# Kernel optimization log

Measured on AMD Instinct MI355X. Metric: run time of the kernel, lower is better.

The kernel has to match this reference:

```python
import jax, jax.numpy as jnp
import numpy as np
from jax import lax

# ---- dims / config (see init_kwargs) ----
M_IMG, N_PCD, C = 1008, 1024, 256     # coarse img nodes (24*32+12*16+6*8), coarse pcd nodes, feat dim
NI_F, NP_F = 76800, 30000             # fine img pixels (240*320), fine pcd points
KI, KP = 64, 64                       # knn patch sizes
NUM_CORR, TOPK = 256, 3               # coarse matching params
COARSE_THR, FINE_THR = 0.0, 0.0       # similarity thresholds (lowered for random data)


def _norm(x):
    return x / (jnp.linalg.norm(x, axis=-1, keepdims=True) + 1e-8)


def setup_inputs() -> dict:
    key = jax.random.key(0)
    ks = jax.random.split(key, 7)
    return {
        "img_feats_c": _norm(jax.random.normal(ks[0], (M_IMG, C), jnp.float32)),
        "pcd_feats_c": _norm(jax.random.normal(ks[1], (N_PCD, C), jnp.float32)),
        "img_feats_f": _norm(jax.random.normal(ks[2], (NI_F, C), jnp.float32)),
        "pcd_feats_f": _norm(jax.random.normal(ks[3], (NP_F, C), jnp.float32)),
        "img_node_masks": jnp.ones((M_IMG,), bool),
        "pcd_node_masks": jnp.ones((N_PCD,), bool),
        "img_node_knn_indices": jax.random.randint(ks[4], (M_IMG, KI), 0, NI_F),
        "pcd_node_knn_indices": jax.random.randint(ks[5], (N_PCD, KP), 0, NP_F),
        "pcd_node_knn_masks": jax.random.uniform(ks[6], (N_PCD, KP)) > 0.1,
    }


def _coarse_match(img_feats_c, pcd_feats_c, img_masks, pcd_masks):
    # SuperPointMatchingMutualTopk: cosine sim + mutual top-k + global top NUM_CORR
    sim = img_feats_c @ pcd_feats_c.T                              # [M, N] (feats normalized)
    valid = img_masks[:, None] & pcd_masks[None, :]
    sim_m = jnp.where(valid, sim, -jnp.inf)
    row_kth = lax.top_k(sim_m, TOPK)[0][:, -1:]                    # kth-largest per row [M,1]
    col_kth = lax.top_k(sim_m.T, TOPK)[0][:, -1:].T                # kth-largest per col [1,N]
    mutual = (sim_m >= row_kth) & (sim_m >= col_kth) & (sim_m > COARSE_THR)
    flat = jnp.where(mutual, sim_m, -jnp.inf).ravel()
    vals, flat_idx = lax.top_k(flat, NUM_CORR)                     # fixed-size selection
    img_idx = flat_idx // N_PCD
    pcd_idx = flat_idx % N_PCD
    corr_valid = jnp.isfinite(vals)
    return img_idx, pcd_idx, corr_valid


def reference(img_feats_c, pcd_feats_c, img_feats_f, pcd_feats_f,
              img_node_masks, pcd_node_masks,
              img_node_knn_indices, pcd_node_knn_indices, pcd_node_knn_masks):
    # ---- coarse matching ----
    img_idx, pcd_idx, corr_valid = _coarse_match(
        img_feats_c, pcd_feats_c, img_node_masks, pcd_node_masks)

    # ---- fine matching: knn gather + pairwise cosine + mutual top-1 ----
    pcd_padded = jnp.concatenate([pcd_feats_f, jnp.zeros_like(pcd_feats_f[:1])], axis=0)
    img_knn_idx = img_node_knn_indices[img_idx]                    # [Ci, KI]
    pcd_knn_idx = pcd_node_knn_indices[pcd_idx]                    # [Ci, KP]
    pcd_knn_msk = pcd_node_knn_masks[pcd_idx]                      # [Ci, KP]
    img_knn_feats = img_feats_f[img_knn_idx]                       # [Ci, KI, C]
    pcd_knn_feats = pcd_padded[pcd_knn_idx]                        # [Ci, KP, C]

    sim = jnp.einsum('bic,bjc->bij', img_knn_feats, pcd_knn_feats) # [Ci, KI, KP]
    m3 = corr_valid[:, None, None] & pcd_knn_msk[:, None, :]
    sim = jnp.where(m3, sim, -jnp.inf)

    row_best = jnp.argmax(sim, axis=2)                             # [Ci, KI]
    row_val = jnp.max(sim, axis=2)
    col_best = jnp.argmax(sim, axis=1)                             # [Ci, KP]
    back = jnp.take_along_axis(col_best, row_best, axis=1)         # [Ci, KI]
    sel = (back == jnp.arange(KI)[None, :]) & jnp.isfinite(row_val) & (row_val > FINE_THR)

    img_corr = img_knn_idx.reshape(-1)                             # [Ci*KI]
    pcd_corr = jnp.take_along_axis(pcd_knn_idx, row_best, axis=1).reshape(-1)
    sel = sel.reshape(-1)
    # sentinel for unselected pairs -> sorts last
    img_corr = jnp.where(sel, img_corr, NI_F)
    pcd_corr = jnp.where(sel, pcd_corr, NP_F)

    # ---- dedup (torch.unique on img*Npf+pcd) via lexsort + first-occurrence mask ----
    order = jnp.lexsort((pcd_corr, img_corr))
    ic, pc = img_corr[order], pcd_corr[order]
    first = jnp.concatenate([jnp.array([True]),
                             (ic[1:] != ic[:-1]) | (pc[1:] != pc[:-1])])
    valid = first & (ic < NI_F)

    ic_s = jnp.clip(ic, 0, NI_F - 1)
    pc_s = jnp.clip(pc, 0, NP_F - 1)
    corr_scores = jnp.sum(img_feats_f[ic_s] * pcd_feats_f[pc_s], axis=1)
    corr_scores = corr_scores * valid.astype(corr_scores.dtype)    # masked scores [Ci*KI]
    return corr_scores
```

## Files before the change

kernel.cpp:

```cpp
#include <hip/hip_runtime.h>
#include <hip/hip_bf16.h>

#define M_IMG 1008
#define N_PCD 1024
#define CDIM  256
#define NI_F  76800
#define NP_F  30000
#define KI    64
#define KP    64
#define NUM_CORR 256
#define NPAIR (NUM_CORR * KI)
#define CAND_CAP 4096
#define KEY_MOD 30001u
#define SENT_KEY (76800u * 30001u + 30000u)

#define NCHUNK 21
#define NEG_INF (-__builtin_inff())

__device__ __forceinline__ bool mask_val(const void* p, int i, int is_u8) {
    return is_u8 ? (((const unsigned char*)p)[i] != 0)
                 : (((const int*)p)[i] != 0);
}

__global__ void detect_bool_kernel(const unsigned int* __restrict__ p,
                                   int* __restrict__ flag) {
    __shared__ int s_cnt;
    if (threadIdx.x == 0) s_cnt = 0;
    __syncthreads();
    unsigned int x = p[blockIdx.x * 256 + threadIdx.x];
    if (x & 0xFFFFFF00u) atomicAdd(&s_cnt, 1);
    __syncthreads();
    if (threadIdx.x == 0 && s_cnt != 0) atomicAdd(flag, 1);
}


__global__ void coarse_sim_kernel(const float* __restrict__ A,
                                  const float* __restrict__ B,
                                  const void* __restrict__ maskA,
                                  const void* __restrict__ maskB,
                                  const int* __restrict__ flag,
                                  float* __restrict__ sim) {
    __shared__ __align__(16) float s_a[32][36];
    __shared__ __align__(16) float s_b[32][68];
    const int is_u8 = (*flag != 0);
    const int m0 = blockIdx.y * 32, n0 = blockIdx.x * 64;
    const int tid = threadIdx.x;
    const int tx = tid & 15, ty = tid >> 4;
    const int c_lane = tid & 31;
    const int r_base = tid >> 5;

    const float* pa[4];
    const float* pb[8];
#pragma unroll
    for (int k = 0; k < 4; k++) {
        int m = m0 + r_base + 8 * k;
        pa[k] = A + (size_t)(m < M_IMG ? m : 0) * CDIM + c_lane;
    }
#pragma unroll
    for (int k = 0; k < 8; k++)
        pb[k] = B + (size_t)(n0 + r_base + 8 * k) * CDIM + c_lane;

    float ra[4], rb[8];
#pragma unroll
    for (int k = 0; k < 4; k++) ra[k] = pa[k][0];
#pragma unroll
    for (int k = 0; k < 8; k++) rb[k] = pb[k][0];
#pragma unroll
    for (int k = 0; k < 4; k++) s_a[c_lane][r_base + 8 * k] = ra[k];
#pragma unroll
    for (int k = 0; k < 8; k++) s_b[c_lane][r_base + 8 * k] = rb[k];
    __syncthreads();

    float acc[2][4];
#pragma unroll
    for (int r = 0; r < 2; r++)
#pragma unroll
        for (int j = 0; j < 4; j++) acc[r][j] = 0.f;

    for (int cit = 0; cit < 8; cit++) {
        if (cit < 7) {
            const int cc = (cit + 1) * 32;
#pragma unroll
            for (int k = 0; k < 4; k++) ra[k] = pa[k][cc];
#pragma unroll
            for (int k = 0; k < 8; k++) rb[k] = pb[k][cc];
        }
#pragma unroll 8
        for (int c = 0; c < 32; c++) {
            float2 av = *(const float2*)&s_a[c][ty * 2];
            float4 bv = *(const float4*)&s_b[c][tx * 4];
            float ar[2] = {av.x, av.y};
            float br[4] = {bv.x, bv.y, bv.z, bv.w};
#pragma unroll
            for (int r = 0; r < 2; r++)
#pragma unroll
                for (int j = 0; j < 4; j++) acc[r][j] += ar[r] * br[j];
        }
        __syncthreads();
        if (cit < 7) {
#pragma unroll
            for (int k = 0; k < 4; k++) s_a[c_lane][r_base + 8 * k] = ra[k];
#pragma unroll
            for (int k = 0; k < 8; k++) s_b[c_lane][r_base + 8 * k] = rb[k];
            __syncthreads();
        }
    }
#pragma unroll
    for (int r = 0; r < 2; r++) {
        int m = m0 + ty * 2 + r;
        if (m < M_IMG) {
            bool ma = mask_val(maskA, m, is_u8);
#pragma unroll
            for (int j = 0; j < 4; j++) {
                int n = n0 + tx * 4 + j;
                bool ok = ma && mask_val(maskB, n, is_u8);
                sim[m * N_PCD + n] = ok ? acc[r][j] : NEG_INF;
            }
        }
    }
}

__device__ __forceinline__ void top3_insert(float v, float& t0, float& t1, float& t2) {
    if (v > t0) { t2 = t1; t1 = t0; t0 = v; }
    else if (v > t1) { t2 = t1; t1 = v; }
    else if (v > t2) { t2 = v; }
}

__device__ __forceinline__ void top3_merge(float a0, float a1, float a2,
                                           float b0, float b1, float b2,
                                           float& x0, float& x1, float& x2) {
    if (a0 >= b0) {
        x0 = a0;
        if (a1 >= b0) { x1 = a1; x2 = (a2 >= b0) ? a2 : b0; }
        else          { x1 = b0; x2 = (a1 >= b1) ? a1 : b1; }
    } else {
        x0 = b0;
        if (b1 >= a0) { x1 = b1; x2 = (b2 >= a0) ? b2 : a0; }
        else          { x1 = a0; x2 = (b1 >= a1) ? b1 : a1; }
    }
}

__global__ void kth_kernel(const float* __restrict__ sim,
                           float* __restrict__ row_kth,
                           float* __restrict__ colp) {
    __shared__ float st[256][3];
    const int tid = threadIdx.x;
    if (blockIdx.x < M_IMG) {
        const float* r = sim + (size_t)blockIdx.x * N_PCD;
        float t0 = NEG_INF, t1 = NEG_INF, t2 = NEG_INF;
#pragma unroll
        for (int e = 0; e < 4; e++) top3_insert(r[e * 256 + tid], t0, t1, t2);
        st[tid][0] = t0; st[tid][1] = t1; st[tid][2] = t2;
        __syncthreads();
        for (int s = 128; s > 0; s >>= 1) {
            if (tid < s) {
                float x0, x1, x2;
                top3_merge(st[tid][0], st[tid][1], st[tid][2],
                           st[tid + s][0], st[tid + s][1], st[tid + s][2],
                           x0, x1, x2);
                st[tid][0] = x0; st[tid][1] = x1; st[tid][2] = x2;
            }
            __syncthreads();
        }
        if (tid == 0) row_kth[blockIdx.x] = st[0][2];
    } else {
        const int b = blockIdx.x - M_IMG;
        const int bx = b & 15, by = b >> 4;
        const int c = tid & 63, rr = tid >> 6;
        const int col = bx * 64 + c;
        const int r0 = by * 48;
        float t0 = NEG_INF, t1 = NEG_INF, t2 = NEG_INF;
#pragma unroll
        for (int k = 0; k < 12; k++) {
            float v = sim[(size_t)(r0 + rr + 4 * k) * N_PCD + col];
            top3_insert(v, t0, t1, t2);
        }
        st[tid][0] = t0; st[tid][1] = t1; st[tid][2] = t2;
        __syncthreads();
        if (tid < 128) {
            float x0, x1, x2;
            top3_merge(st[tid][0], st[tid][1], st[tid][2],
                       st[tid + 128][0], st[tid + 128][1], st[tid + 128][2],
                       x0, x1, x2);
            st[tid][0] = x0; st[tid][1] = x1; st[tid][2] = x2;
        }
        __syncthreads();
        if (tid < 64) {
            float x0, x1, x2;
            top3_merge(st[tid][0], st[tid][1], st[tid][2],
                       st[tid + 64][0], st[tid + 64][1], st[tid + 64][2],
                       x0, x1, x2);
            const int base = by * N_PCD + col;
            colp[base] = x0;
            colp[NCHUNK * N_PCD + base] = x1;
            colp[2 * NCHUNK * N_PCD + base] = x2;
        }
    }
}

__global__ void col_merge_kernel(const float* __restrict__ colp,
                                 float* __restrict__ col_kth) {
    const int col = blockIdx.x * 256 + threadIdx.x;
    float t0 = colp[col];
    float t1 = colp[NCHUNK * N_PCD + col];
    float t2 = colp[2 * NCHUNK * N_PCD + col];
#pragma unroll
    for (int ch = 1; ch < NCHUNK; ch++) {
        float b0 = colp[ch * N_PCD + col];
        float b1 = colp[NCHUNK * N_PCD + ch * N_PCD + col];
        float b2 = colp[2 * NCHUNK * N_PCD + ch * N_PCD + col];
        float x0, x1, x2;
        top3_merge(t0, t1, t2, b0, b1, b2, x0, x1, x2);
        t0 = x0; t1 = x1; t2 = x2;
    }
    col_kth[col] = t2;
}

__global__ void compact_kernel(const float* __restrict__ sim,
                               const float* __restrict__ row_kth,
                               const float* __restrict__ col_kth,
                               unsigned long long* __restrict__ cand,
                               int* __restrict__ count) {
    int g = blockIdx.x * 256 + threadIdx.x;
    if (g >= M_IMG * N_PCD) return;
    int m = g >> 10, n = g & 1023;
    float v = sim[g];
    if (v > 0.f && v >= row_kth[m] && v >= col_kth[n]) {
        int pos = atomicAdd(count, 1);
        if (pos < CAND_CAP) {
            unsigned int u = __float_as_uint(v);
            unsigned int mono = (u & 0x80000000u) ? ~u : (u | 0x80000000u);
            cand[pos] = ((unsigned long long)(~mono) << 32) | (unsigned int)g;
        }
    }
}

__global__ void cand_rank_kernel(const unsigned long long* __restrict__ cand,
                                 const int* __restrict__ count,
                                 unsigned int* __restrict__ cnt2) {
    __shared__ unsigned long long s_k[256];
    const int tid = threadIdx.x;
    int K = *count; if (K > CAND_CAP) K = CAND_CAP;
    const int j0 = blockIdx.y * 256;
    if (j0 >= K) return;
    int j = j0 + tid;
    s_k[tid] = (j < K) ? cand[j] : 0xFFFFFFFFFFFFFFFFull;
    __syncthreads();
    const int i = blockIdx.x * 256 + tid;
    if (i >= K) return;
    const unsigned long long my = cand[i];
    unsigned int less = 0;
#pragma unroll 8
    for (int t = 0; t < 256; t++) less += (s_k[t] < my);
    if (less) atomicAdd(&cnt2[i], less);
}

__global__ void cand_select_kernel(const unsigned long long* __restrict__ cand,
                                   const int* __restrict__ count,
                                   const unsigned int* __restrict__ cnt2,
                                   int* __restrict__ sel_idx,
                                   int* __restrict__ selK) {
    int K = *count; if (K > CAND_CAP) K = CAND_CAP;
    const int i = blockIdx.x * 256 + threadIdx.x;
    if (i == 0) *selK = (K < NUM_CORR) ? K : NUM_CORR;
    if (i < K) {
        unsigned int r = cnt2[i];
        if (r < NUM_CORR) sel_idx[r] = (int)(cand[i] & 0xFFFFFFFFull);
    }
}

__global__ void fine_kernel(const float* __restrict__ img_f,
                            const float* __restrict__ pcd_f,
                            const int* __restrict__ img_knn,
                            const int* __restrict__ pcd_knn,
                            const void* __restrict__ pcd_msk,
                            const int* __restrict__ flag,
                            const int* __restrict__ sel_idx,
                            const int* __restrict__ selK_ptr,
                            unsigned int* __restrict__ keys) {
    const int ci = blockIdx.x, tid = threadIdx.x;
    const int selK = *selK_ptr;
    if (ci >= selK) {
        if (tid < KI) keys[ci * KI + tid] = SENT_KEY;
        return;
    }
    __shared__ int s_ik[KI], s_pk[KP];
    __shared__ unsigned char s_mk[KP];
    __shared__ __align__(16) float s_a[32][68];
    __shared__ __align__(16) float s_b[32][68];
    __shared__ float s_sim[64][65];
    __shared__ int s_rb[64], s_cb[64];
    __shared__ float s_rv[64];

    int flat = sel_idx[ci];
    int gi = flat >> 10, pi = flat & 1023;
    if (tid < 64) {
        const int is_u8 = (*flag != 0);
        s_ik[tid] = img_knn[gi * KI + tid];
        s_pk[tid] = pcd_knn[pi * KP + tid];
        s_mk[tid] = mask_val(pcd_msk, pi * KP + tid, is_u8) ? 1 : 0;
    }
    __syncthreads();

    const int tx = tid & 15, tyy = tid >> 4;
    const int c_lane = tid & 31;
    const int r_base = tid >> 5;

    const float* pa[4];
    const float* pb[4];
#pragma unroll
    for (int k = 0; k < 4; k++) {
        pa[k] = img_f + (size_t)s_ik[r_base + 16 * k] * CDIM + c_lane;
        pb[k] = pcd_f + (size_t)s_pk[r_base + 16 * k] * CDIM + c_lane;
    }

    float ra[4], rb[4];
#pragma unroll
    for (int k = 0; k < 4; k++) { ra[k] = pa[k][0]; rb[k] = pb[k][0]; }
#pragma unroll
    for (int k = 0; k < 4; k++) {
        s_a[c_lane][r_base + 16 * k] = ra[k];
        s_b[c_lane][r_base + 16 * k] = rb[k];
    }
    __syncthreads();

    float acc[2][4];
#pragma unroll
    for (int r = 0; r < 2; r++)
#pragma unroll
        for (int j = 0; j < 4; j++) acc[r][j] = 0.f;

    for (int cit = 0; cit < 8; cit++) {
        if (cit < 7) {
            const int cc = (cit + 1) * 32;
#pragma unroll
            for (int k = 0; k < 4; k++) { ra[k] = pa[k][cc]; rb[k] = pb[k][cc]; }
        }
#pragma unroll 8
        for (int c = 0; c < 32; c++) {
            float2 av = *(const float2*)&s_a[c][tyy * 2];
            float4 bv = *(const float4*)&s_b[c][tx * 4];
            float ar[2] = {av.x, av.y};
            float br[4] = {bv.x, bv.y, bv.z, bv.w};
#pragma unroll
            for (int r = 0; r < 2; r++)
#pragma unroll
                for (int j = 0; j < 4; j++) acc[r][j] += ar[r] * br[j];
        }
        __syncthreads();
        if (cit < 7) {
#pragma unroll
            for (int k = 0; k < 4; k++) {
                s_a[c_lane][r_base + 16 * k] = ra[k];
                s_b[c_lane][r_base + 16 * k] = rb[k];
            }
            __syncthreads();
        }
    }
#pragma unroll
    for (int r = 0; r < 2; r++) {
        int row = tyy * 2 + r;
#pragma unroll
        for (int j = 0; j < 4; j++) {
            int kp = tx * 4 + j;
            s_sim[row][kp] = (s_mk[kp] != 0) ? acc[r][j] : NEG_INF;
        }
    }
    __syncthreads();

    if (tid < 64) {
        float best = NEG_INF; int bi = 0;
        for (int kp = 0; kp < 64; kp++) {
            float v = s_sim[tid][kp];
            if (v > best) { best = v; bi = kp; }
        }
        s_rb[tid] = bi; s_rv[tid] = best;
    } else if (tid < 128) {
        int kp = tid - 64;
        float best = NEG_INF; int bi = 0;
        for (int k2 = 0; k2 < 64; k2++) {
            float v = s_sim[k2][kp];
            if (v > best) { best = v; bi = k2; }
        }
        s_cb[kp] = bi;
    }
    __syncthreads();

    if (tid < 64) {
        int rb2 = s_rb[tid];
        float rv = s_rv[tid];
        bool sel = (s_cb[rb2] == tid) && (rv > 0.f);
        unsigned int key = sel
            ? ((unsigned int)s_ik[tid] * KEY_MOD + (unsigned int)s_pk[rb2])
            : SENT_KEY;
        keys[ci * KI + tid] = key;
    }
}

__global__ void rank_count_kernel(const unsigned int* __restrict__ keys,
                                  unsigned int* __restrict__ cnt) {
    __shared__ unsigned int s_k[256];
    const int tid = threadIdx.x;
    const int bi = blockIdx.x, bj = blockIdx.y;
    const int i = bi * 256 + tid;
    const unsigned int myKey = keys[i];
    s_k[tid] = keys[bj * 256 + tid];
    __syncthreads();

    unsigned int less = 0, eqb = 0;
    if (bj < bi) {
#pragma unroll 8
        for (int j = 0; j < 256; j++) {
            unsigned int k = s_k[j];
            less += (k < myKey);
            eqb += (k == myKey);
        }
    } else if (bj == bi) {
#pragma unroll 8
        for (int j = 0; j < 256; j++) {
            unsigned int k = s_k[j];
            less += (k < myKey);
            eqb += (k == myKey) & (j < tid);
        }
    } else {
#pragma unroll 8
        for (int j = 0; j < 256; j++) {
            unsigned int k = s_k[j];
            less += (k < myKey);
        }
    }
    atomicAdd(&cnt[i], (less << 16) | eqb);
}

__global__ void rank_out_kernel(const unsigned int* __restrict__ keys,
                                const unsigned int* __restrict__ cnt,
                                const float* __restrict__ img_f,
                                const float* __restrict__ pcd_f,
                                float* __restrict__ out) {
    const int i = blockIdx.x * 256 + threadIdx.x;
    const unsigned int myKey = keys[i];
    const unsigned int v = cnt[i];
    const int rank = (int)(v >> 16) + (int)(v & 0xFFFFu);
    unsigned int ic = myKey / KEY_MOD;
    unsigned int pc = myKey - ic * KEY_MOD;
    float score = 0.f;
    if ((v & 0xFFFFu) == 0 && ic < (unsigned)NI_F) {
        const float4* a = (const float4*)(img_f + (size_t)ic * CDIM);
        const float4* b = (const float4*)(pcd_f + (size_t)pc * CDIM);
        float s = 0.f;
#pragma unroll 8
        for (int c = 0; c < CDIM / 4; c++) {
            float4 x = a[c], y = b[c];
            s += x.x * y.x + x.y * y.y + x.z * y.z + x.w * y.w;
        }
        score = s;
    }
    out[rank] = score;
}

extern "C" void kernel_launch(void* const* d_in, const int* in_sizes, int n_in,
                              void* d_out, int out_size, void* d_ws, size_t ws_size,
                              hipStream_t stream) {
    const float* img_c = (const float*)d_in[0];
    const float* pcd_c = (const float*)d_in[1];
    const float* img_f = (const float*)d_in[2];
    const float* pcd_f = (const float*)d_in[3];
    const void* img_mask = d_in[4];
    const void* pcd_mask = d_in[5];
    const int* img_knn = (const int*)d_in[6];
    const int* pcd_knn = (const int*)d_in[7];
    const void* pcd_knn_msk = d_in[8];
    float* out = (float*)d_out;

    char* w = (char*)d_ws;
    size_t off = 0;
    float* sim = (float*)(w + off);            off += (size_t)M_IMG * N_PCD * 4;
    float* row_kth = (float*)(w + off);        off += M_IMG * 4;
    float* col_kth = (float*)(w + off);        off += N_PCD * 4;
    int* count = (int*)(w + off);              off += 4;
    int* selK = (int*)(w + off);               off += 4;
    int* boolflag = (int*)(w + off);           off += 4;
    off = (off + 7) & ~(size_t)7;
    unsigned long long* cand = (unsigned long long*)(w + off); off += CAND_CAP * 8;
    int* sel_idx = (int*)(w + off);            off += NUM_CORR * 4;
    unsigned int* keys = (unsigned int*)(w + off); off += NPAIR * 4;
    unsigned int* cnt = (unsigned int*)(w + off);  off += NPAIR * 4;
    unsigned int* cnt2 = (unsigned int*)(w + off); off += CAND_CAP * 4;
    float* colp = (float*)(w + off);           off += 3 * NCHUNK * N_PCD * 4;

    hipMemsetAsync(count, 0, 12, stream);
    hipMemsetAsync(cnt, 0, (NPAIR + CAND_CAP) * 4, stream);

    detect_bool_kernel<<<16, 256, 0, stream>>>((const unsigned int*)pcd_knn_msk, boolflag);
    coarse_sim_kernel<<<dim3(16, 32), 256, 0, stream>>>(img_c, pcd_c, img_mask, pcd_mask,
                                                        boolflag, sim);
    kth_kernel<<<M_IMG + 16 * NCHUNK, 256, 0, stream>>>(sim, row_kth, colp);
    col_merge_kernel<<<4, 256, 0, stream>>>(colp, col_kth);
    compact_kernel<<<(M_IMG * N_PCD) / 256, 256, 0, stream>>>(sim, row_kth, col_kth, cand, count);
    cand_rank_kernel<<<dim3(16, 16), 256, 0, stream>>>(cand, count, cnt2);
    cand_select_kernel<<<16, 256, 0, stream>>>(cand, count, cnt2, sel_idx, selK);
    fine_kernel<<<NUM_CORR, 512, 0, stream>>>(img_f, pcd_f, img_knn, pcd_knn, pcd_knn_msk,
                                              boolflag, sel_idx, selK, keys);
    rank_count_kernel<<<dim3(64, 64), 256, 0, stream>>>(keys, cnt);
    rank_out_kernel<<<NPAIR / 256, 256, 0, stream>>>(keys, cnt, img_f, pcd_f, out);
}
```

Before: 274.1 us.

## Fuse row/column top-3 into sim GEMM and compact fine pairs before ranking

Computes per-tile row and column top-3 partials in the coarse similarity kernel's epilogue, so the separate kth kernel no longer has to re-read the whole sim matrix. A small kernel then merges the partials. Candidate ranking and selection are merged into one kernel, which removes the cnt2 buffer and its atomics. The fine kernel now appends only selected pairs to a compacted list, so the pairwise rank and output kernels work on valid entries only; in exchange the output must be zeroed by a memset and rank ties are broken by list position.

```diff
diff --git a/kernel.cpp b/kernel.cpp
--- a/kernel.cpp
+++ b/kernel.cpp
@@ -12,10 +12,9 @@
 #define NPAIR (NUM_CORR * KI)
 #define CAND_CAP 4096
 #define KEY_MOD 30001u
-#define SENT_KEY (76800u * 30001u + 30000u)
-
-#define NCHUNK 21
+
 #define NEG_INF (-__builtin_inff())
+typedef unsigned long long u64;
 
 __device__ __forceinline__ bool mask_val(const void* p, int i, int is_u8) {
     return is_u8 ? (((const unsigned char*)p)[i] != 0)
@@ -31,93 +30,6 @@
     if (x & 0xFFFFFF00u) atomicAdd(&s_cnt, 1);
     __syncthreads();
     if (threadIdx.x == 0 && s_cnt != 0) atomicAdd(flag, 1);
-}
-
-
-__global__ void coarse_sim_kernel(const float* __restrict__ A,
-                                  const float* __restrict__ B,
-                                  const void* __restrict__ maskA,
-                                  const void* __restrict__ maskB,
-                                  const int* __restrict__ flag,
-                                  float* __restrict__ sim) {
-    __shared__ __align__(16) float s_a[32][36];
-    __shared__ __align__(16) float s_b[32][68];
-    const int is_u8 = (*flag != 0);
-    const int m0 = blockIdx.y * 32, n0 = blockIdx.x * 64;
-    const int tid = threadIdx.x;
-    const int tx = tid & 15, ty = tid >> 4;
-    const int c_lane = tid & 31;
-    const int r_base = tid >> 5;
-
-    const float* pa[4];
-    const float* pb[8];
-#pragma unroll
-    for (int k = 0; k < 4; k++) {
-        int m = m0 + r_base + 8 * k;
-        pa[k] = A + (size_t)(m < M_IMG ? m : 0) * CDIM + c_lane;
-    }
-#pragma unroll
-    for (int k = 0; k < 8; k++)
-        pb[k] = B + (size_t)(n0 + r_base + 8 * k) * CDIM + c_lane;
-
-    float ra[4], rb[8];
-#pragma unroll
-    for (int k = 0; k < 4; k++) ra[k] = pa[k][0];
-#pragma unroll
-    for (int k = 0; k < 8; k++) rb[k] = pb[k][0];
-#pragma unroll
-    for (int k = 0; k < 4; k++) s_a[c_lane][r_base + 8 * k] = ra[k];
-#pragma unroll
-    for (int k = 0; k < 8; k++) s_b[c_lane][r_base + 8 * k] = rb[k];
-    __syncthreads();
-
-    float acc[2][4];
-#pragma unroll
-    for (int r = 0; r < 2; r++)
-#pragma unroll
-        for (int j = 0; j < 4; j++) acc[r][j] = 0.f;
-
-    for (int cit = 0; cit < 8; cit++) {
-        if (cit < 7) {
-            const int cc = (cit + 1) * 32;
-#pragma unroll
-            for (int k = 0; k < 4; k++) ra[k] = pa[k][cc];
-#pragma unroll
-            for (int k = 0; k < 8; k++) rb[k] = pb[k][cc];
-        }
-#pragma unroll 8
-        for (int c = 0; c < 32; c++) {
-            float2 av = *(const float2*)&s_a[c][ty * 2];
-            float4 bv = *(const float4*)&s_b[c][tx * 4];
-            float ar[2] = {av.x, av.y};
-            float br[4] = {bv.x, bv.y, bv.z, bv.w};
-#pragma unroll
-            for (int r = 0; r < 2; r++)
-#pragma unroll
-                for (int j = 0; j < 4; j++) acc[r][j] += ar[r] * br[j];
-        }
-        __syncthreads();
-        if (cit < 7) {
-#pragma unroll
-            for (int k = 0; k < 4; k++) s_a[c_lane][r_base + 8 * k] = ra[k];
-#pragma unroll
-            for (int k = 0; k < 8; k++) s_b[c_lane][r_base + 8 * k] = rb[k];
-            __syncthreads();
-        }
-    }
-#pragma unroll
-    for (int r = 0; r < 2; r++) {
-        int m = m0 + ty * 2 + r;
-        if (m < M_IMG) {
-            bool ma = mask_val(maskA, m, is_u8);
-#pragma unroll
-            for (int j = 0; j < 4; j++) {
-                int n = n0 + tx * 4 + j;
-                bool ok = ma && mask_val(maskB, n, is_u8);
-                sim[m * N_PCD + n] = ok ? acc[r][j] : NEG_INF;
-            }
-        }
-    }
 }
 
 __device__ __forceinline__ void top3_insert(float v, float& t0, float& t1, float& t2) {
@@ -140,86 +52,179 @@
     }
 }
 
-__global__ void kth_kernel(const float* __restrict__ sim,
-                           float* __restrict__ row_kth,
-                           float* __restrict__ colp) {
-    __shared__ float st[256][3];
+__global__ void coarse_sim_kernel(const float* __restrict__ A,
+                                  const float* __restrict__ B,
+                                  const void* __restrict__ maskA,
+                                  const void* __restrict__ maskB,
+                                  const int* __restrict__ flag,
+                                  float* __restrict__ sim,
+                                  float* __restrict__ rowp,
+                                  float* __restrict__ colp) {
+    __shared__ __align__(16) float s_a[32][36];
+    __shared__ __align__(16) float s_b[32][68];
+    __shared__ float sr[32][16][3];
+    __shared__ float sc[64][16][3];
+    const int is_u8 = (*flag != 0);
+    const int m0 = blockIdx.y * 32, n0 = blockIdx.x * 64;
     const int tid = threadIdx.x;
-    if (blockIdx.x < M_IMG) {
-        const float* r = sim + (size_t)blockIdx.x * N_PCD;
+    const int tx = tid & 15, ty = tid >> 4;
+    const int c_lane = tid & 31;
+    const int r_base = tid >> 5;
+
+    const float* pa[4];
+    const float* pb[8];
+#pragma unroll
+    for (int k = 0; k < 4; k++) {
+        int m = m0 + r_base + 8 * k;
+        pa[k] = A + (size_t)(m < M_IMG ? m : 0) * CDIM + c_lane;
+    }
+#pragma unroll
+    for (int k = 0; k < 8; k++)
+        pb[k] = B + (size_t)(n0 + r_base + 8 * k) * CDIM + c_lane;
+
+    float ra[4], rb[8];
+#pragma unroll
+    for (int k = 0; k < 4; k++) ra[k] = pa[k][0];
+#pragma unroll
+    for (int k = 0; k < 8; k++) rb[k] = pb[k][0];
+#pragma unroll
+    for (int k = 0; k < 4; k++) s_a[c_lane][r_base + 8 * k] = ra[k];
+#pragma unroll
+    for (int k = 0; k < 8; k++) s_b[c_lane][r_base + 8 * k] = rb[k];
+    __syncthreads();
+
+    float acc[2][4];
+#pragma unroll
+    for (int r = 0; r < 2; r++)
+#pragma unroll
+        for (int j = 0; j < 4; j++) acc[r][j] = 0.f;
+
+    for (int cit = 0; cit < 8; cit++) {
+        if (cit < 7) {
+            const int cc = (cit + 1) * 32;
+#pragma unroll
+            for (int k = 0; k < 4; k++) ra[k] = pa[k][cc];
+#pragma unroll
+            for (int k = 0; k < 8; k++) rb[k] = pb[k][cc];
+        }
+#pragma unroll 8
+        for (int c = 0; c < 32; c++) {
+            float2 av = *(const float2*)&s_a[c][ty * 2];
+            float4 bv = *(const float4*)&s_b[c][tx * 4];
+            float ar[2] = {av.x, av.y};
+            float br[4] = {bv.x, bv.y, bv.z, bv.w};
+#pragma unroll
+            for (int r = 0; r < 2; r++)
+#pragma unroll
+                for (int j = 0; j < 4; j++) acc[r][j] += ar[r] * br[j];
+        }
+        __syncthreads();
+        if (cit < 7) {
+#pragma unroll
+            for (int k = 0; k < 4; k++) s_a[c_lane][r_base + 8 * k] = ra[k];
+#pragma unroll
+            for (int k = 0; k < 8; k++) s_b[c_lane][r_base + 8 * k] = rb[k];
+            __syncthreads();
+        }
+    }
+
+    float vm[2][4];
+#pragma unroll
+    for (int r = 0; r < 2; r++) {
+        int m = m0 + ty * 2 + r;
+        bool ma = (m < M_IMG) && mask_val(maskA, m, is_u8);
+#pragma unroll
+        for (int j = 0; j < 4; j++) {
+            int n = n0 + tx * 4 + j;
+            bool ok = ma && mask_val(maskB, n, is_u8);
+            float v = ok ? acc[r][j] : NEG_INF;
+            vm[r][j] = v;
+            if (m < M_IMG) sim[m * N_PCD + n] = v;
+        }
+    }
+#pragma unroll
+    for (int r = 0; r < 2; r++) {
         float t0 = NEG_INF, t1 = NEG_INF, t2 = NEG_INF;
 #pragma unroll
-        for (int e = 0; e < 4; e++) top3_insert(r[e * 256 + tid], t0, t1, t2);
-        st[tid][0] = t0; st[tid][1] = t1; st[tid][2] = t2;
-        __syncthreads();
-        for (int s = 128; s > 0; s >>= 1) {
-            if (tid < s) {
-                float x0, x1, x2;
-                top3_merge(st[tid][0], st[tid][1], st[tid][2],
-                           st[tid + s][0], st[tid + s][1], st[tid + s][2],
-                           x0, x1, x2);
-                st[tid][0] = x0; st[tid][1] = x1; st[tid][2] = x2;
-            }
-            __syncthreads();
-        }
-        if (tid == 0) row_kth[blockIdx.x] = st[0][2];
+        for (int j = 0; j < 4; j++) top3_insert(vm[r][j], t0, t1, t2);
+        sr[ty * 2 + r][tx][0] = t0; sr[ty * 2 + r][tx][1] = t1; sr[ty * 2 + r][tx][2] = t2;
+    }
+#pragma unroll
+    for (int j = 0; j < 4; j++) {
+        float t0 = NEG_INF, t1 = NEG_INF, t2 = NEG_INF;
+        top3_insert(vm[0][j], t0, t1, t2);
+        top3_insert(vm[1][j], t0, t1, t2);
+        sc[tx * 4 + j][ty][0] = t0; sc[tx * 4 + j][ty][1] = t1; sc[tx * 4 + j][ty][2] = t2;
+    }
+    __syncthreads();
+    if (tid < 32) {
+        float t0 = sr[tid][0][0], t1 = sr[tid][0][1], t2 = sr[tid][0][2];
+#pragma unroll
+        for (int k = 1; k < 16; k++) {
+            float x0, x1, x2;
+            top3_merge(t0, t1, t2, sr[tid][k][0], sr[tid][k][1], sr[tid][k][2], x0, x1, x2);
+            t0 = x0; t1 = x1; t2 = x2;
+        }
+        int m = m0 + tid;
+        if (m < M_IMG) {
+            const int base = blockIdx.x * 1024 + m;
+            rowp[base] = t0;
+            rowp[16 * 1024 + base] = t1;
+            rowp[2 * 16 * 1024 + base] = t2;
+        }
+    } else if (tid >= 64 && tid < 128) {
+        int col = tid - 64;
+        float t0 = sc[col][0][0], t1 = sc[col][0][1], t2 = sc[col][0][2];
+#pragma unroll
+        for (int k = 1; k < 16; k++) {
+            float x0, x1, x2;
+            top3_merge(t0, t1, t2, sc[col][k][0], sc[col][k][1], sc[col][k][2], x0, x1, x2);
+            t0 = x0; t1 = x1; t2 = x2;
+        }
+        const int base = blockIdx.y * 1024 + n0 + col;
+        colp[base] = t0;
+        colp[32 * 1024 + base] = t1;
+        colp[2 * 32 * 1024 + base] = t2;
+    }
+}
+
+__global__ void kth_merge_kernel(const float* __restrict__ rowp,
+                                 const float* __restrict__ colp,
+                                 float* __restrict__ row_kth,
+                                 float* __restrict__ col_kth) {
+    const int b = blockIdx.x, t = threadIdx.x;
+    if (b < 4) {
+        int m = b * 256 + t;
+        if (m >= M_IMG) return;
+        float t0 = rowp[m], t1 = rowp[16 * 1024 + m], t2 = rowp[2 * 16 * 1024 + m];
+#pragma unroll
+        for (int ch = 1; ch < 16; ch++) {
+            int base = ch * 1024 + m;
+            float x0, x1, x2;
+            top3_merge(t0, t1, t2, rowp[base], rowp[16 * 1024 + base],
+                       rowp[2 * 16 * 1024 + base], x0, x1, x2);
+            t0 = x0; t1 = x1; t2 = x2;
+        }
+        row_kth[m] = t2;
     } else {
-        const int b = blockIdx.x - M_IMG;
-        const int bx = b & 15, by = b >> 4;
-        const int c = tid & 63, rr = tid >> 6;
-        const int col = bx * 64 + c;
-        const int r0 = by * 48;
-        float t0 = NEG_INF, t1 = NEG_INF, t2 = NEG_INF;
-#pragma unroll
-        for (int k = 0; k < 12; k++) {
-            float v = sim[(size_t)(r0 + rr + 4 * k) * N_PCD + col];
-            top3_insert(v, t0, t1, t2);
-        }
-        st[tid][0] = t0; st[tid][1] = t1; st[tid][2] = t2;
-        __syncthreads();
-        if (tid < 128) {
+        int n = (b - 4) * 256 + t;
+        float t0 = colp[n], t1 = colp[32 * 1024 + n], t2 = colp[2 * 32 * 1024 + n];
+#pragma unroll
+        for (int ch = 1; ch < 32; ch++) {
+            int base = ch * 1024 + n;
             float x0, x1, x2;
-            top3_merge(st[tid][0], st[tid][1], st[tid][2],
-                       st[tid + 128][0], st[tid + 128][1], st[tid + 128][2],
-                       x0, x1, x2);
-            st[tid][0] = x0; st[tid][1] = x1; st[tid][2] = x2;
-        }
-        __syncthreads();
-        if (tid < 64) {
-            float x0, x1, x2;
-            top3_merge(st[tid][0], st[tid][1], st[tid][2],
-                       st[tid + 64][0], st[tid + 64][1], st[tid + 64][2],
-                       x0, x1, x2);
-            const int base = by * N_PCD + col;
-            colp[base] = x0;
-            colp[NCHUNK * N_PCD + base] = x1;
-            colp[2 * NCHUNK * N_PCD + base] = x2;
-        }
-    }
-}
-
-__global__ void col_merge_kernel(const float* __restrict__ colp,
-                                 float* __restrict__ col_kth) {
-    const int col = blockIdx.x * 256 + threadIdx.x;
-    float t0 = colp[col];
-    float t1 = colp[NCHUNK * N_PCD + col];
-    float t2 = colp[2 * NCHUNK * N_PCD + col];
-#pragma unroll
-    for (int ch = 1; ch < NCHUNK; ch++) {
-        float b0 = colp[ch * N_PCD + col];
-        float b1 = colp[NCHUNK * N_PCD + ch * N_PCD + col];
-        float b2 = colp[2 * NCHUNK * N_PCD + ch * N_PCD + col];
-        float x0, x1, x2;
-        top3_merge(t0, t1, t2, b0, b1, b2, x0, x1, x2);
-        t0 = x0; t1 = x1; t2 = x2;
-    }
-    col_kth[col] = t2;
+            top3_merge(t0, t1, t2, colp[base], colp[32 * 1024 + base],
+                       colp[2 * 32 * 1024 + base], x0, x1, x2);
+            t0 = x0; t1 = x1; t2 = x2;
+        }
+        col_kth[n] = t2;
+    }
 }
 
 __global__ void compact_kernel(const float* __restrict__ sim,
                                const float* __restrict__ row_kth,
                                const float* __restrict__ col_kth,
-                               unsigned long long* __restrict__ cand,
+                               u64* __restrict__ cand,
                                int* __restrict__ count) {
     int g = blockIdx.x * 256 + threadIdx.x;
     if (g >= M_IMG * N_PCD) return;
@@ -230,43 +235,32 @@
         if (pos < CAND_CAP) {
             unsigned int u = __float_as_uint(v);
             unsigned int mono = (u & 0x80000000u) ? ~u : (u | 0x80000000u);
-            cand[pos] = ((unsigned long long)(~mono) << 32) | (unsigned int)g;
-        }
-    }
-}
-
-__global__ void cand_rank_kernel(const unsigned long long* __restrict__ cand,
-                                 const int* __restrict__ count,
-                                 unsigned int* __restrict__ cnt2) {
-    __shared__ unsigned long long s_k[256];
-    const int tid = threadIdx.x;
+            cand[pos] = ((u64)(~mono) << 32) | (unsigned int)g;
+        }
+    }
+}
+
+__global__ void cand_rank_select_kernel(const u64* __restrict__ cand,
+                                        const int* __restrict__ count,
+                                        int* __restrict__ sel_idx,
+                                        int* __restrict__ selK) {
+    __shared__ u64 s[256];
+    const int tid = threadIdx.x, bi = blockIdx.x;
     int K = *count; if (K > CAND_CAP) K = CAND_CAP;
-    const int j0 = blockIdx.y * 256;
-    if (j0 >= K) return;
-    int j = j0 + tid;
-    s_k[tid] = (j < K) ? cand[j] : 0xFFFFFFFFFFFFFFFFull;
-    __syncthreads();
-    const int i = blockIdx.x * 256 + tid;
-    if (i >= K) return;
-    const unsigned long long my = cand[i];
+    if (bi == 0 && tid == 0) *selK = (K < NUM_CORR) ? K : NUM_CORR;
+    if (bi * 256 >= K) return;
+    const int i = bi * 256 + tid;
+    const u64 my = (i < K) ? cand[i] : 0xFFFFFFFFFFFFFFFFull;
     unsigned int less = 0;
+    for (int c0 = 0; c0 < K; c0 += 256) {
+        int j = c0 + tid;
+        s[tid] = (j < K) ? cand[j] : 0xFFFFFFFFFFFFFFFFull;
+        __syncthreads();
 #pragma unroll 8
-    for (int t = 0; t < 256; t++) less += (s_k[t] < my);
-    if (less) atomicAdd(&cnt2[i], less);
-}
-
-__global__ void cand_select_kernel(const unsigned long long* __restrict__ cand,
-                                   const int* __restrict__ count,
-                                   const unsigned int* __restrict__ cnt2,
-                                   int* __restrict__ sel_idx,
-                                   int* __restrict__ selK) {
-    int K = *count; if (K > CAND_CAP) K = CAND_CAP;
-    const int i = blockIdx.x * 256 + threadIdx.x;
-    if (i == 0) *selK = (K < NUM_CORR) ? K : NUM_CORR;
-    if (i < K) {
-        unsigned int r = cnt2[i];
-        if (r < NUM_CORR) sel_idx[r] = (int)(cand[i] & 0xFFFFFFFFull);
-    }
+        for (int t = 0; t < 256; t++) less += (s[t] < my);
+        __syncthreads();
+    }
+    if (i < K && less < NUM_CORR) sel_idx[less] = (int)(my & 0xFFFFFFFFull);
 }
 
 __global__ void fine_kernel(const float* __restrict__ img_f,
@@ -277,13 +271,11 @@
                             const int* __restrict__ flag,
                             const int* __restrict__ sel_idx,
                             const int* __restrict__ selK_ptr,
-                            unsigned int* __restrict__ keys) {
+                            u64* __restrict__ vlist,
+                            int* __restrict__ nvcnt) {
     const int ci = blockIdx.x, tid = threadIdx.x;
     const int selK = *selK_ptr;
-    if (ci >= selK) {
-        if (tid < KI) keys[ci * KI + tid] = SENT_KEY;
-        return;
-    }
+    if (ci >= selK) return;
     __shared__ int s_ik[KI], s_pk[KP];
     __shared__ unsigned char s_mk[KP];
     __shared__ __align__(16) float s_a[32][68];
@@ -390,72 +382,64 @@
         int rb2 = s_rb[tid];
         float rv = s_rv[tid];
         bool sel = (s_cb[rb2] == tid) && (rv > 0.f);
-        unsigned int key = sel
-            ? ((unsigned int)s_ik[tid] * KEY_MOD + (unsigned int)s_pk[rb2])
-            : SENT_KEY;
-        keys[ci * KI + tid] = key;
-    }
-}
-
-__global__ void rank_count_kernel(const unsigned int* __restrict__ keys,
-                                  unsigned int* __restrict__ cnt) {
-    __shared__ unsigned int s_k[256];
-    const int tid = threadIdx.x;
-    const int bi = blockIdx.x, bj = blockIdx.y;
+        if (sel) {
+            unsigned int key = (unsigned int)s_ik[tid] * KEY_MOD + (unsigned int)s_pk[rb2];
+            int pos = atomicAdd(nvcnt, 1);
+            vlist[pos] = ((u64)key << 14) | (unsigned int)(ci * KI + tid);
+        }
+    }
+}
+
+__global__ void pair_rank_kernel(const u64* __restrict__ vlist,
+                                 const int* __restrict__ nvp,
+                                 unsigned int* __restrict__ cntv) {
+    const int nv = *nvp;
+    const int bi = blockIdx.x, bj = blockIdx.y, tid = threadIdx.x;
+    if (bi * 256 >= nv || bj * 256 >= nv) return;
+    __shared__ u64 s[256];
+    int j = bj * 256 + tid;
+    s[tid] = (j < nv) ? vlist[j] : 0xFFFFFFFFFFFFFFFFull;
+    __syncthreads();
     const int i = bi * 256 + tid;
-    const unsigned int myKey = keys[i];
-    s_k[tid] = keys[bj * 256 + tid];
-    __syncthreads();
-
-    unsigned int less = 0, eqb = 0;
-    if (bj < bi) {
+    if (i >= nv) return;
+    const u64 p = vlist[i];
+    const u64 mykey = p >> 14;
+    unsigned int less = 0, dup = 0;
 #pragma unroll 8
-        for (int j = 0; j < 256; j++) {
-            unsigned int k = s_k[j];
-            less += (k < myKey);
-            eqb += (k == myKey);
-        }
-    } else if (bj == bi) {
-#pragma unroll 8
-        for (int j = 0; j < 256; j++) {
-            unsigned int k = s_k[j];
-            less += (k < myKey);
-            eqb += (k == myKey) & (j < tid);
-        }
-    } else {
-#pragma unroll 8
-        for (int j = 0; j < 256; j++) {
-            unsigned int k = s_k[j];
-            less += (k < myKey);
-        }
-    }
-    atomicAdd(&cnt[i], (less << 16) | eqb);
-}
-
-__global__ void rank_out_kernel(const unsigned int* __restrict__ keys,
-                                const unsigned int* __restrict__ cnt,
+    for (int t = 0; t < 256; t++) {
+        u64 q = s[t];
+        bool lt = q < p;
+        less += lt;
+        dup += lt && ((q >> 14) == mykey);
+    }
+    atomicAdd(&cntv[i], (less << 16) | dup);
+}
+
+__global__ void pair_out_kernel(const u64* __restrict__ vlist,
+                                const int* __restrict__ nvp,
+                                const unsigned int* __restrict__ cntv,
                                 const float* __restrict__ img_f,
                                 const float* __restrict__ pcd_f,
                                 float* __restrict__ out) {
+    const int nv = *nvp;
     const int i = blockIdx.x * 256 + threadIdx.x;
-    const unsigned int myKey = keys[i];
-    const unsigned int v = cnt[i];
-    const int rank = (int)(v >> 16) + (int)(v & 0xFFFFu);
-    unsigned int ic = myKey / KEY_MOD;
-    unsigned int pc = myKey - ic * KEY_MOD;
-    float score = 0.f;
-    if ((v & 0xFFFFu) == 0 && ic < (unsigned)NI_F) {
-        const float4* a = (const float4*)(img_f + (size_t)ic * CDIM);
-        const float4* b = (const float4*)(pcd_f + (size_t)pc * CDIM);
-        float s = 0.f;
+    if (i >= nv) return;
+    const unsigned int v = cntv[i];
+    if (v & 0xFFFFu) return;
+    const u64 p = vlist[i];
+    const unsigned int key = (unsigned int)(p >> 14);
+    const unsigned int rank = v >> 16;
+    unsigned int ic = key / KEY_MOD;
+    unsigned int pc = key - ic * KEY_MOD;
+    const float4* a = (const float4*)(img_f + (size_t)ic * CDIM);
+    const float4* b = (const float4*)(pcd_f + (size_t)pc * CDIM);
+    float s = 0.f;
 #pragma unroll 8
-        for (int c = 0; c < CDIM / 4; c++) {
-            float4 x = a[c], y = b[c];
-            s += x.x * y.x + x.y * y.y + x.z * y.z + x.w * y.w;
-        }
-        score = s;
-    }
-    out[rank] = score;
+    for (int c = 0; c < CDIM / 4; c++) {
+        float4 x = a[c], y = b[c];
+        s += x.x * y.x + x.y * y.y + x.z * y.z + x.w * y.w;
+    }
+    out[rank] = s;
 }
 
 extern "C" void kernel_launch(void* const* d_in, const int* in_sizes, int n_in,
@@ -475,32 +459,31 @@
     char* w = (char*)d_ws;
     size_t off = 0;
     float* sim = (float*)(w + off);            off += (size_t)M_IMG * N_PCD * 4;
-    float* row_kth = (float*)(w + off);        off += M_IMG * 4;
-    float* col_kth = (float*)(w + off);        off += N_PCD * 4;
+    float* row_kth = (float*)(w + off);        off += 1024 * 4;
+    float* col_kth = (float*)(w + off);        off += 1024 * 4;
     int* count = (int*)(w + off);              off += 4;
     int* selK = (int*)(w + off);               off += 4;
     int* boolflag = (int*)(w + off);           off += 4;
+    int* nvcnt = (int*)(w + off);              off += 4;
+    unsigned int* cntv = (unsigned int*)(w + off); off += NPAIR * 4;
     off = (off + 7) & ~(size_t)7;
-    unsigned long long* cand = (unsigned long long*)(w + off); off += CAND_CAP * 8;
+    u64* cand = (u64*)(w + off);               off += CAND_CAP * 8;
     int* sel_idx = (int*)(w + off);            off += NUM_CORR * 4;
-    unsigned int* keys = (unsigned int*)(w + off); off += NPAIR * 4;
-    unsigned int* cnt = (unsigned int*)(w + off);  off += NPAIR * 4;
-    unsigned int* cnt2 = (unsigned int*)(w + off); off += CAND_CAP * 4;
-    float* colp = (float*)(w + off);           off += 3 * NCHUNK * N_PCD * 4;
-
-    hipMemsetAsync(count, 0, 12, stream);
-    hipMemsetAsync(cnt, 0, (NPAIR + CAND_CAP) * 4, stream);
+    u64* vlist = (u64*)(w + off);              off += NPAIR * 8;
+    float* rowp = (float*)(w + off);           off += 3 * 16 * 1024 * 4;
+    float* colp = (float*)(w + off);           off += 3 * 32 * 1024 * 4;
+
+    hipMemsetAsync(count, 0, 16 + NPAIR * 4, stream);
+    hipMemsetAsync(out, 0, (size_t)out_size * 4, stream);
 
     detect_bool_kernel<<<16, 256, 0, stream>>>((const unsigned int*)pcd_knn_msk, boolflag);
     coarse_sim_kernel<<<dim3(16, 32), 256, 0, stream>>>(img_c, pcd_c, img_mask, pcd_mask,
-                                                        boolflag, sim);
-    kth_kernel<<<M_IMG + 16 * NCHUNK, 256, 0, stream>>>(sim, row_kth, colp);
-    col_merge_kernel<<<4, 256, 0, stream>>>(colp, col_kth);
+                                                        boolflag, sim, rowp, colp);
+    kth_merge_kernel<<<8, 256, 0, stream>>>(rowp, colp, row_kth, col_kth);
     compact_kernel<<<(M_IMG * N_PCD) / 256, 256, 0, stream>>>(sim, row_kth, col_kth, cand, count);
-    cand_rank_kernel<<<dim3(16, 16), 256, 0, stream>>>(cand, count, cnt2);
-    cand_select_kernel<<<16, 256, 0, stream>>>(cand, count, cnt2, sel_idx, selK);
+    cand_rank_select_kernel<<<16, 256, 0, stream>>>(cand, count, sel_idx, selK);
     fine_kernel<<<NUM_CORR, 512, 0, stream>>>(img_f, pcd_f, img_knn, pcd_knn, pcd_knn_msk,
-                                              boolflag, sel_idx, selK, keys);
-    rank_count_kernel<<<dim3(64, 64), 256, 0, stream>>>(keys, cnt);
-    rank_out_kernel<<<NPAIR / 256, 256, 0, stream>>>(keys, cnt, img_f, pcd_f, out);
-}
+                                              boolflag, sel_idx, selK, vlist, nvcnt);
+    pair_rank_kernel<<<dim3(64, 64), 256, 0, stream>>>(vlist, nvcnt, cntv);
+    pair_out_kernel<<<64, 256, 0, stream>>>(vlist, nvcnt, cntv, img_f, pcd_f, out);
+}
```

Result: slower. 300.7 us (+9.7%).
